# Kernel tuning notes

Hardware: AMD Instinct MI355X
Metric: run time of the kernel (lower is better)

## Reference

```python
import jax, jax.numpy as jnp
import numpy as np

EPS_DIV = 1e-7   # matches .div(sigma + 1e-07) and denominator + 1e-07
EPS_NORM = 1e-12  # torch F.normalize default eps


def setup_inputs() -> dict:
    key = jax.random.key(0)
    k1, k2, k3, k4 = jax.random.split(key, 4)
    B, C, H, W = 4, 128, 64, 64
    K = 32
    stdv = 1.0 / np.sqrt(C)
    return {
        "x": jax.random.normal(k1, (B, C, H, W), dtype=jnp.float32),
        "anchor": jax.random.uniform(k2, (K, C), dtype=jnp.float32),
        "sigma_param": jax.random.uniform(k3, (K, C), dtype=jnp.float32),
        "gcn_weight": jax.random.uniform(k4, (C, C), dtype=jnp.float32,
                                         minval=-stdv, maxval=stdv),
    }


def _l2_normalize(v, axis):
    n = jnp.sqrt(jnp.sum(v * v, axis=axis, keepdims=True))
    return v / jnp.maximum(n, EPS_NORM)


def reference(x, anchor, sigma_param, gcn_weight):
    B, C, H, W = x.shape
    N = H * W
    K = anchor.shape[0]

    # --- GraphNet (NetVLAD-style soft assignment pooling) ---
    sigma = jax.nn.sigmoid(sigma_param)                        # [K, C]
    xf = x.reshape(B, C, N).transpose(0, 2, 1)                 # [B, N, C]
    # residual: [B, K, N, C]
    residual = (xf[:, None, :, :] - anchor[None, :, None, :]) / (
        sigma[None, :, None, :] + EPS_DIV)
    logits = -0.5 * jnp.sum(residual * residual, axis=3)       # [B, K, N]
    soft_assign = jax.nn.softmax(logits, axis=1)               # softmax over nodes K

    numerator = jnp.einsum('bknc,bkn->bkc', residual, soft_assign)  # [B, K, C]
    denominator = jnp.sum(soft_assign, axis=2)[..., None]           # [B, K, 1]
    nodes = numerator / (denominator + EPS_DIV)                     # [B, K, C]

    nodes = _l2_normalize(nodes, axis=2)
    flat = nodes.reshape(B, -1)
    flat = _l2_normalize(flat, axis=1)
    graph = flat.reshape(B, C, K)  # note: pure reshape as in torch .view

    # --- CascadeGCNet, loop = 1 ---
    adj = jnp.einsum('bck,bcl->bkl', graph, graph)             # x_t @ x -> [B, K, K]
    adj = jax.nn.softmax(adj, axis=2)
    support = jnp.einsum('bck,cd->bkd', graph, gcn_weight)     # [B, K, C]
    graph = jnp.einsum('bkl,bld->bkd', adj, support).transpose(0, 2, 1)  # [B, C, K]
    graph = jax.nn.relu(graph)

    # --- project back ---
    out = jnp.einsum('bck,bkn->bcn', graph, soft_assign)       # [B, C, N]
    return out.reshape(B, C, H, W)
```

## Files before the change

kernel.cpp:

```cpp
#include <hip/hip_runtime.h>
#include <math.h>

#define BB 4
#define CC 128
#define KK 32
#define NN 4096
#define NSL 64

__launch_bounds__(1024, 4)
__global__ void k_A(const float* __restrict__ x, const float* __restrict__ anchor,
                    const float* __restrict__ sigp, float* __restrict__ sa,
                    float* __restrict__ pnum, float* __restrict__ pden) {
  const int b  = blockIdx.y, s = blockIdx.x;
  const int n0 = s * 64;
  const int t  = threadIdx.x;
  const int lane = t & 63;
  const int w  = __builtin_amdgcn_readfirstlane(t >> 6);

  __shared__ float  xt[CC][68];
  __shared__ float4 wt4[16][129];
  __shared__ float  plg[4][64][36];
  __shared__ float  stK[KK][68];
  __shared__ float  ckL[KK];
  __shared__ float  pdenP[8][36];

  {
#pragma unroll
    for (int e = 0; e < 2; e++) {
      int i = t + e * 1024;
      int c = i >> 4, pq = i & 15;
      float4 v = *(const float4*)(x + ((size_t)b * CC + c) * NN + n0 + 4 * pq);
      *(float4*)&xt[c][4 * pq] = v;
    }
  }

  {
    const int kp = w;
    const int k0 = kp * 2, k1 = k0 + 1;
    float s0 = 0.f, s1 = 0.f;
#pragma unroll
    for (int e = 0; e < 2; e++) {
      int c = lane * 2 + e;
      float sp0 = sigp[k0 * CC + c], sp1 = sigp[k1 * CC + c];
      float a0  = anchor[k0 * CC + c], a1 = anchor[k1 * CC + c];
      float sg0 = 1.0f / (1.0f + expf(-sp0));
      float sg1 = 1.0f / (1.0f + expf(-sp1));
      float iv0 = 1.0f / (sg0 + 1e-7f), iv1 = 1.0f / (sg1 + 1e-7f);
      float w20 = iv0 * iv0, w21 = iv1 * iv1;
      wt4[kp][c] = make_float4(w20, -2.0f * a0 * w20, w21, -2.0f * a1 * w21);
      s0 = fmaf(a0 * a0, w20, s0);
      s1 = fmaf(a1 * a1, w21, s1);
    }
#pragma unroll
    for (int d = 1; d < 64; d <<= 1) {
      s0 += __shfl_xor(s0, d);
      s1 += __shfl_xor(s1, d);
    }
    if (lane == 0) { ckL[k0] = s0; ckL[k1] = s1; }
  }
  __syncthreads();

  {
    const int px4 = t & 15, kp = (t >> 4) & 15, ch = t >> 8;
    float acc[4][2];
#pragma unroll
    for (int i = 0; i < 4; i++) { acc[i][0] = 0.f; acc[i][1] = 0.f; }
    for (int c0 = 0; c0 < 32; c0++) {
      const int c = ch * 32 + c0;
      float4 xv = *(const float4*)&xt[c][px4 * 4];
      float4 wv = wt4[kp][c];
#pragma unroll
      for (int i = 0; i < 4; i++) {
        float xs = (&xv.x)[i];
        acc[i][0] = fmaf(xs, fmaf(xs, wv.x, wv.y), acc[i][0]);
        acc[i][1] = fmaf(xs, fmaf(xs, wv.z, wv.w), acc[i][1]);
      }
    }
#pragma unroll
    for (int i = 0; i < 4; i++) {
      plg[ch][px4 * 4 + i][kp * 2 + 0] = acc[i][0];
      plg[ch][px4 * 4 + i][kp * 2 + 1] = acc[i][1];
    }
  }
  __syncthreads();

  if (t < 512) {
    const int p  = w * 8 + (lane >> 3);
    const int kq = lane & 7;
    float4 l0  = *(float4*)&plg[0][p][kq * 4];
    float4 l1  = *(float4*)&plg[1][p][kq * 4];
    float4 l2  = *(float4*)&plg[2][p][kq * 4];
    float4 l3  = *(float4*)&plg[3][p][kq * 4];
    float4 ckv = *(float4*)&ckL[kq * 4];
    float4 lv;
    lv.x = -0.5f * (l0.x + l1.x + l2.x + l3.x + ckv.x);
    lv.y = -0.5f * (l0.y + l1.y + l2.y + l3.y + ckv.y);
    lv.z = -0.5f * (l0.z + l1.z + l2.z + l3.z + ckv.z);
    lv.w = -0.5f * (l0.w + l1.w + l2.w + l3.w + ckv.w);
    float m = fmaxf(fmaxf(lv.x, lv.y), fmaxf(lv.z, lv.w));
    m = fmaxf(m, __shfl_xor(m, 1));
    m = fmaxf(m, __shfl_xor(m, 2));
    m = fmaxf(m, __shfl_xor(m, 4));
    float e0 = __expf(lv.x - m), e1 = __expf(lv.y - m);
    float e2 = __expf(lv.z - m), e3 = __expf(lv.w - m);
    float sum = e0 + e1 + e2 + e3;
    sum += __shfl_xor(sum, 1);
    sum += __shfl_xor(sum, 2);
    sum += __shfl_xor(sum, 4);
    float rs = 1.0f / sum;
    e0 *= rs; e1 *= rs; e2 *= rs; e3 *= rs;
    stK[kq * 4 + 0][p] = e0;
    stK[kq * 4 + 1][p] = e1;
    stK[kq * 4 + 2][p] = e2;
    stK[kq * 4 + 3][p] = e3;
    float p0 = e0, p1 = e1, p2 = e2, p3 = e3;
    p0 += __shfl_xor(p0, 8);  p1 += __shfl_xor(p1, 8);
    p2 += __shfl_xor(p2, 8);  p3 += __shfl_xor(p3, 8);
    p0 += __shfl_xor(p0, 16); p1 += __shfl_xor(p1, 16);
    p2 += __shfl_xor(p2, 16); p3 += __shfl_xor(p3, 16);
    p0 += __shfl_xor(p0, 32); p1 += __shfl_xor(p1, 32);
    p2 += __shfl_xor(p2, 32); p3 += __shfl_xor(p3, 32);
    if (lane < 8) {
      pdenP[w][lane * 4 + 0] = p0;
      pdenP[w][lane * 4 + 1] = p1;
      pdenP[w][lane * 4 + 2] = p2;
      pdenP[w][lane * 4 + 3] = p3;
    }
  }
  __syncthreads();

  if (t < KK) {
    float d = 0.f;
#pragma unroll
    for (int ww = 0; ww < 8; ww++) d += pdenP[ww][t];
    pden[((size_t)b * NSL + s) * KK + t] = d;
  }

  if (t < 512) {
    const int k = t >> 4, j4 = t & 15;
    float4 v = *(float4*)&stK[k][4 * j4];
    *(float4*)(sa + ((size_t)b * KK + k) * NN + n0 + 4 * j4) = v;
  }

  {
    const int k = t & 31, cg = t >> 5;
    float acc[4];
#pragma unroll
    for (int i = 0; i < 4; i++) acc[i] = 0.f;
    const float* xb = x + (size_t)(b * CC + cg * 4) * NN + n0;
    for (int j4 = 0; j4 < 16; j4++) {
      float4 sv = *(float4*)&stK[k][4 * j4];
#pragma unroll
      for (int i = 0; i < 4; i++) {
        float4 xr = *(const float4*)(xb + (size_t)i * NN + 4 * j4);
        acc[i] = fmaf(sv.x, xr.x, acc[i]);
        acc[i] = fmaf(sv.y, xr.y, acc[i]);
        acc[i] = fmaf(sv.z, xr.z, acc[i]);
        acc[i] = fmaf(sv.w, xr.w, acc[i]);
      }
    }
    float* pp = pnum + (((size_t)b * NSL + s) * KK + k) * CC + cg * 4;
    *(float4*)pp = make_float4(acc[0], acc[1], acc[2], acc[3]);
  }
}

__launch_bounds__(256)
__global__ void k_red(const float* __restrict__ pnum, const float* __restrict__ pden,
                      const float* __restrict__ sigp, const float* __restrict__ anchor,
                      float* __restrict__ nodes, float* __restrict__ n1sq) {
  const int t = threadIdx.x;
  const int g = blockIdx.x * 256 + t;
  const int c = g & 127, k = (g >> 7) & 31, b = g >> 12;

  float dk = 0.0f;
#pragma unroll 8
  for (int s = 0; s < NSL; s++) dk += pden[((size_t)b * NSL + s) * KK + k];

  float q = 0.0f;
#pragma unroll 8
  for (int s = 0; s < NSL; s++)
    q += pnum[(((size_t)b * NSL + s) * KK + k) * CC + c];

  const int idx = k * CC + c;
  float sg = 1.0f / (1.0f + expf(-sigp[idx]));
  float iv = 1.0f / (sg + 1e-7f);
  float val = iv * (q - anchor[idx] * dk) / (dk + 1e-7f);
  nodes[((size_t)b * KK + k) * CC + c] = val;

  __shared__ float red[256];
  red[t] = val * val;
  __syncthreads();
  for (int sft = 64; sft > 0; sft >>= 1) {
    if ((t & 127) < sft) red[t] += red[t + sft];
    __syncthreads();
  }
  if ((t & 127) == 0) n1sq[b * KK + k] = red[t];
}

__launch_bounds__(1024, 4)
__global__ void k_BC(const float* __restrict__ nodes, const float* __restrict__ n1sq,
                     const float* __restrict__ W, const float* __restrict__ sa,
                     float* __restrict__ out) {
  const int b = blockIdx.y, s = blockIdx.x;
  const int n0 = s * 64;
  const int t = threadIdx.x;
  __shared__ float flat[KK * CC];
  __shared__ float sup[KK][130];
  __shared__ float adjm[KK][33];
  __shared__ float gbL[CC][KK + 1];
  __shared__ float n1v[KK], nsq[KK];
  __shared__ float n2s;

  const int k = t >> 5, cq = t & 31;
  float4 val = ((const float4*)(nodes + (size_t)b * KK * CC))[k * 32 + cq];

  if (t < KK) {
    float s2 = n1sq[b * KK + t];
    float n1 = fmaxf(sqrtf(s2), 1e-12f);
    n1v[t] = n1;
    nsq[t] = s2 / (n1 * n1);
  }
  __syncthreads();
  if (t == 0) {
    float tot = 0.0f;
#pragma unroll
    for (int kk = 0; kk < KK; kk++) tot += nsq[kk];
    n2s = fmaxf(sqrtf(tot), 1e-12f);
  }
  __syncthreads();
  {
    float sc = 1.0f / (n1v[k] * n2s);
    val.x *= sc; val.y *= sc; val.z *= sc; val.w *= sc;
    ((float4*)flat)[k * 32 + cq] = val;
  }
  __syncthreads();

  {
    const int k2 = t >> 5, l = t & 31;
    float a = 0.0f;
#pragma unroll 8
    for (int i = 0; i < CC; i++)
      a = fmaf(flat[i * KK + k2], flat[i * KK + l], a);
    adjm[k2][l] = a;
  }
  __syncthreads();
  if (t < KK) {
    float m = -1e30f;
#pragma unroll
    for (int l = 0; l < KK; l++) m = fmaxf(m, adjm[t][l]);
    float s2 = 0.0f;
#pragma unroll
    for (int l = 0; l < KK; l++) { float e = __expf(adjm[t][l] - m); adjm[t][l] = e; s2 += e; }
    float r = 1.0f / s2;
#pragma unroll
    for (int l = 0; l < KK; l++) adjm[t][l] *= r;
  }
  __syncthreads();

  {
    const int d = t & 127, lg = t >> 7;
    float sacc[4] = {0.0f, 0.0f, 0.0f, 0.0f};
    for (int c = 0; c < CC; c++) {
      float wv = W[c * CC + d];
#pragma unroll
      for (int j = 0; j < 4; j++)
        sacc[j] = fmaf(flat[c * KK + lg + 8 * j], wv, sacc[j]);
    }
#pragma unroll
    for (int j = 0; j < 4; j++) sup[lg + 8 * j][d] = sacc[j];
  }
  __syncthreads();

  {
    const int d = t & 127, lg = t >> 7;
#pragma unroll
    for (int j = 0; j < 4; j++) {
      int kk = lg + 8 * j;
      float g = 0.0f;
#pragma unroll
      for (int l = 0; l < KK; l++) g = fmaf(adjm[kk][l], sup[l][d], g);
      gbL[d][kk] = fmaxf(g, 0.0f);
    }
  }
  __syncthreads();

  {
    const int nl = t & 63, cw = t >> 6;
    const int c0 = cw * 8;
    float sreg[KK];
    const float* spt = sa + (size_t)b * KK * NN + n0 + nl;
#pragma unroll
    for (int kk = 0; kk < KK; kk++) sreg[kk] = spt[(size_t)kk * NN];

    float* op = out + ((size_t)b * CC + c0) * NN + n0 + nl;
#pragma unroll
    for (int ci = 0; ci < 8; ci++) {
      float acc = 0.0f;
#pragma unroll
      for (int kk = 0; kk < KK; kk++)
        acc = fmaf(gbL[c0 + ci][kk], sreg[kk], acc);
      op[(size_t)ci * NN] = acc;
    }
  }
}

extern "C" void kernel_launch(void* const* d_in, const int* in_sizes, int n_in,
                              void* d_out, int out_size, void* d_ws, size_t ws_size,
                              hipStream_t stream) {
  const float* x      = (const float*)d_in[0];
  const float* anchor = (const float*)d_in[1];
  const float* sigp   = (const float*)d_in[2];
  const float* W      = (const float*)d_in[3];
  float* out = (float*)d_out;

  float* ws    = (float*)d_ws;
  float* pden  = ws;
  float* pnum  = ws + 8192;
  float* nodes = ws + 1056768;
  float* n1sq  = ws + 1073152;
  float* sa    = ws + 1073280;

  k_A  <<<dim3(NSL, BB), dim3(1024), 0, stream>>>(x, anchor, sigp, sa, pnum, pden);
  k_red<<<dim3(64),      dim3(256),  0, stream>>>(pnum, pden, sigp, anchor, nodes, n1sq);
  k_BC <<<dim3(NSL, BB), dim3(1024), 0, stream>>>(nodes, n1sq, W, sa, out);
}
```

Measured before the change: 54.29 us.

## Register-tile logits and numerator GEMMs in k_A using transposed LDS copies

The logits stage now uses 256 threads, each computing an 8-pixel by 4-node register tile. The numerator stage reads a transposed x tile and transposed soft-assign from LDS instead of re-reading x from global memory, with 128 threads each computing an 8x8 tile. Partial numerators are now split into two halves per slice, which doubles the pnum workspace and the reduction length in k_red. Most threads sit idle in both compute phases, and the extra LDS buffers, possible bank conflicts on the transposed stores and larger partial-sum traffic may offset the gain from reuse.

Result: slower. 58.11 us (+7.0%).

```diff
diff --git a/kernel.cpp b/kernel.cpp
--- a/kernel.cpp
+++ b/kernel.cpp
@@ -6,6 +6,7 @@
 #define KK 32
 #define NN 4096
 #define NSL 64
+#define NSL2 128
 
 __launch_bounds__(1024, 4)
 __global__ void k_A(const float* __restrict__ x, const float* __restrict__ anchor,
@@ -17,12 +18,14 @@
   const int lane = t & 63;
   const int w  = __builtin_amdgcn_readfirstlane(t >> 6);
 
-  __shared__ float  xt[CC][68];
-  __shared__ float4 wt4[16][129];
-  __shared__ float  plg[4][64][36];
-  __shared__ float  stK[KK][68];
-  __shared__ float  ckL[KK];
-  __shared__ float  pdenP[8][36];
+  __shared__ __align__(16) float  xt[CC][64];
+  __shared__ __align__(16) float  xtT[64][132];
+  __shared__ __align__(16) float4 wt4[16][129];
+  __shared__ __align__(16) float  plg[4][64][36];
+  __shared__ __align__(16) float  stT[64][36];
+  __shared__ __align__(16) float  stK[KK][68];
+  __shared__ __align__(16) float  ckL[KK];
+  __shared__ float pdenP[8][36];
 
   {
 #pragma unroll
@@ -31,6 +34,10 @@
       int c = i >> 4, pq = i & 15;
       float4 v = *(const float4*)(x + ((size_t)b * CC + c) * NN + n0 + 4 * pq);
       *(float4*)&xt[c][4 * pq] = v;
+      xtT[4 * pq + 0][c] = v.x;
+      xtT[4 * pq + 1][c] = v.y;
+      xtT[4 * pq + 2][c] = v.z;
+      xtT[4 * pq + 3][c] = v.w;
     }
   }
 
@@ -60,27 +67,42 @@
   }
   __syncthreads();
 
-  {
-    const int px4 = t & 15, kp = (t >> 4) & 15, ch = t >> 8;
-    float acc[4][2];
-#pragma unroll
-    for (int i = 0; i < 4; i++) { acc[i][0] = 0.f; acc[i][1] = 0.f; }
+  if (t < 256) {
+    const int cs = w;
+    const int pxg = lane & 7, kg = lane >> 3;
+    float acc[8][4];
+#pragma unroll
+    for (int i = 0; i < 8; i++)
+#pragma unroll
+      for (int j = 0; j < 4; j++) acc[i][j] = 0.f;
+
     for (int c0 = 0; c0 < 32; c0++) {
-      const int c = ch * 32 + c0;
-      float4 xv = *(const float4*)&xt[c][px4 * 4];
-      float4 wv = wt4[kp][c];
+      const int c = cs * 32 + c0;
+      float4 xv0 = *(float4*)&xt[c][pxg * 8];
+      float4 xv1 = *(float4*)&xt[c][pxg * 8 + 4];
+      float4 w0  = wt4[kg * 2][c];
+      float4 w1  = wt4[kg * 2 + 1][c];
 #pragma unroll
       for (int i = 0; i < 4; i++) {
-        float xs = (&xv.x)[i];
-        acc[i][0] = fmaf(xs, fmaf(xs, wv.x, wv.y), acc[i][0]);
-        acc[i][1] = fmaf(xs, fmaf(xs, wv.z, wv.w), acc[i][1]);
+        float xs = (&xv0.x)[i];
+        acc[i][0] = fmaf(xs, fmaf(xs, w0.x, w0.y), acc[i][0]);
+        acc[i][1] = fmaf(xs, fmaf(xs, w0.z, w0.w), acc[i][1]);
+        acc[i][2] = fmaf(xs, fmaf(xs, w1.x, w1.y), acc[i][2]);
+        acc[i][3] = fmaf(xs, fmaf(xs, w1.z, w1.w), acc[i][3]);
       }
-    }
-#pragma unroll
-    for (int i = 0; i < 4; i++) {
-      plg[ch][px4 * 4 + i][kp * 2 + 0] = acc[i][0];
-      plg[ch][px4 * 4 + i][kp * 2 + 1] = acc[i][1];
-    }
+#pragma unroll
+      for (int i = 0; i < 4; i++) {
+        float xs = (&xv1.x)[i];
+        acc[4 + i][0] = fmaf(xs, fmaf(xs, w0.x, w0.y), acc[4 + i][0]);
+        acc[4 + i][1] = fmaf(xs, fmaf(xs, w0.z, w0.w), acc[4 + i][1]);
+        acc[4 + i][2] = fmaf(xs, fmaf(xs, w1.x, w1.y), acc[4 + i][2]);
+        acc[4 + i][3] = fmaf(xs, fmaf(xs, w1.z, w1.w), acc[4 + i][3]);
+      }
+    }
+#pragma unroll
+    for (int i = 0; i < 8; i++)
+      *(float4*)&plg[cs][pxg * 8 + i][kg * 4] =
+          make_float4(acc[i][0], acc[i][1], acc[i][2], acc[i][3]);
   }
   __syncthreads();
 
@@ -109,6 +131,7 @@
     sum += __shfl_xor(sum, 4);
     float rs = 1.0f / sum;
     e0 *= rs; e1 *= rs; e2 *= rs; e3 *= rs;
+    *(float4*)&stT[p][kq * 4] = make_float4(e0, e1, e2, e3);
     stK[kq * 4 + 0][p] = e0;
     stK[kq * 4 + 1][p] = e1;
     stK[kq * 4 + 2][p] = e2;
@@ -142,25 +165,37 @@
     *(float4*)(sa + ((size_t)b * KK + k) * NN + n0 + 4 * j4) = v;
   }
 
-  {
-    const int k = t & 31, cg = t >> 5;
-    float acc[4];
-#pragma unroll
-    for (int i = 0; i < 4; i++) acc[i] = 0.f;
-    const float* xb = x + (size_t)(b * CC + cg * 4) * NN + n0;
-    for (int j4 = 0; j4 < 16; j4++) {
-      float4 sv = *(float4*)&stK[k][4 * j4];
-#pragma unroll
-      for (int i = 0; i < 4; i++) {
-        float4 xr = *(const float4*)(xb + (size_t)i * NN + 4 * j4);
-        acc[i] = fmaf(sv.x, xr.x, acc[i]);
-        acc[i] = fmaf(sv.y, xr.y, acc[i]);
-        acc[i] = fmaf(sv.z, xr.z, acc[i]);
-        acc[i] = fmaf(sv.w, xr.w, acc[i]);
-      }
-    }
-    float* pp = pnum + (((size_t)b * NSL + s) * KK + k) * CC + cg * 4;
-    *(float4*)pp = make_float4(acc[0], acc[1], acc[2], acc[3]);
+  if (t >= 512 && t < 640) {
+    const int tt = t - 512;
+    const int kg = tt & 3;
+    const int cg = (tt >> 2) & 15;
+    const int ns = tt >> 6;
+    float acc[8][8];
+#pragma unroll
+    for (int i = 0; i < 8; i++)
+#pragma unroll
+      for (int j = 0; j < 8; j++) acc[i][j] = 0.f;
+
+    for (int p0 = 0; p0 < 32; p0++) {
+      const int px = ns * 32 + p0;
+      float4 s0 = *(float4*)&stT[px][kg * 8];
+      float4 s1 = *(float4*)&stT[px][kg * 8 + 4];
+      float4 x0 = *(float4*)&xtT[px][cg * 8];
+      float4 x1 = *(float4*)&xtT[px][cg * 8 + 4];
+      float sk[8] = {s0.x, s0.y, s0.z, s0.w, s1.x, s1.y, s1.z, s1.w};
+      float xc[8] = {x0.x, x0.y, x0.z, x0.w, x1.x, x1.y, x1.z, x1.w};
+#pragma unroll
+      for (int i = 0; i < 8; i++)
+#pragma unroll
+        for (int j = 0; j < 8; j++)
+          acc[i][j] = fmaf(sk[i], xc[j], acc[i][j]);
+    }
+#pragma unroll
+    for (int i = 0; i < 8; i++) {
+      float* pp = pnum + (((size_t)b * NSL2 + s * 2 + ns) * KK + kg * 8 + i) * CC + cg * 8;
+      *(float4*)pp       = make_float4(acc[i][0], acc[i][1], acc[i][2], acc[i][3]);
+      *(float4*)(pp + 4) = make_float4(acc[i][4], acc[i][5], acc[i][6], acc[i][7]);
+    }
   }
 }
 
@@ -178,8 +213,8 @@
 
   float q = 0.0f;
 #pragma unroll 8
-  for (int s = 0; s < NSL; s++)
-    q += pnum[(((size_t)b * NSL + s) * KK + k) * CC + c];
+  for (int s = 0; s < NSL2; s++)
+    q += pnum[(((size_t)b * NSL2 + s) * KK + k) * CC + c];
 
   const int idx = k * CC + c;
   float sg = 1.0f / (1.0f + expf(-sigp[idx]));
@@ -316,9 +351,9 @@
   float* ws    = (float*)d_ws;
   float* pden  = ws;
   float* pnum  = ws + 8192;
-  float* nodes = ws + 1056768;
-  float* n1sq  = ws + 1073152;
-  float* sa    = ws + 1073280;
+  float* nodes = ws + 2105344;
+  float* n1sq  = ws + 2121728;
+  float* sa    = ws + 2121856;
 
   k_A  <<<dim3(NSL, BB), dim3(1024), 0, stream>>>(x, anchor, sigp, sa, pnum, pden);
   k_red<<<dim3(64),      dim3(256),  0, stream>>>(pnum, pden, sigp, anchor, nodes, n1sq);
```

## Halve k_A pixel slice to 32 with 512-thread blocks, doubling slice count

Applied to the files above, without the earlier changes.

The first kernel now processes 32 pixels per block with 512 threads instead of 64 pixels with 1024, so it launches twice as many blocks (128 slices per batch). The per-node constant reduction changes from wave shuffles to a shared-memory partial sum. The numerator loop now has each thread accumulate 8 channels. The intent is better occupancy and more blocks across CUs. The cost is doubling the partial-sum buffers that k_red must reduce over, while k_BC keeps its own 64-slice grid.

After: 68.42 us. 1.26x slower.

```diff
diff --git a/kernel.cpp b/kernel.cpp
--- a/kernel.cpp
+++ b/kernel.cpp
@@ -5,42 +5,45 @@
 #define CC 128
 #define KK 32
 #define NN 4096
-#define NSL 64
-
-__launch_bounds__(1024, 4)
+#define PX 32
+#define NSL 128
+#define NSLB 64
+
+__launch_bounds__(512, 4)
 __global__ void k_A(const float* __restrict__ x, const float* __restrict__ anchor,
                     const float* __restrict__ sigp, float* __restrict__ sa,
                     float* __restrict__ pnum, float* __restrict__ pden) {
   const int b  = blockIdx.y, s = blockIdx.x;
-  const int n0 = s * 64;
+  const int n0 = s * PX;
   const int t  = threadIdx.x;
   const int lane = t & 63;
   const int w  = __builtin_amdgcn_readfirstlane(t >> 6);
 
-  __shared__ float  xt[CC][68];
-  __shared__ float4 wt4[16][129];
-  __shared__ float  plg[4][64][36];
-  __shared__ float  stK[KK][68];
-  __shared__ float  ckL[KK];
-  __shared__ float  pdenP[8][36];
+  __shared__ __align__(16) float  xt[CC][36];
+  __shared__ __align__(16) float4 wt4[16][128];
+  __shared__ __align__(16) float  plg[4][PX][36];
+  __shared__ __align__(16) float  stK[KK][36];
+  __shared__ __align__(16) float  ckp[KK][33];
+  __shared__ __align__(16) float  ckL[KK];
+  __shared__ float pdenP[4][36];
 
   {
 #pragma unroll
     for (int e = 0; e < 2; e++) {
-      int i = t + e * 1024;
-      int c = i >> 4, pq = i & 15;
+      int i = t + e * 512;
+      int c = i >> 3, pq = i & 7;
       float4 v = *(const float4*)(x + ((size_t)b * CC + c) * NN + n0 + 4 * pq);
       *(float4*)&xt[c][4 * pq] = v;
     }
   }
 
   {
-    const int kp = w;
+    const int kp = t >> 5;
     const int k0 = kp * 2, k1 = k0 + 1;
     float s0 = 0.f, s1 = 0.f;
 #pragma unroll
-    for (int e = 0; e < 2; e++) {
-      int c = lane * 2 + e;
+    for (int e = 0; e < 4; e++) {
+      int c = ((t * 4) + e) & 127;
       float sp0 = sigp[k0 * CC + c], sp1 = sigp[k1 * CC + c];
       float a0  = anchor[k0 * CC + c], a1 = anchor[k1 * CC + c];
       float sg0 = 1.0f / (1.0f + expf(-sp0));
@@ -51,17 +54,20 @@
       s0 = fmaf(a0 * a0, w20, s0);
       s1 = fmaf(a1 * a1, w21, s1);
     }
-#pragma unroll
-    for (int d = 1; d < 64; d <<= 1) {
-      s0 += __shfl_xor(s0, d);
-      s1 += __shfl_xor(s1, d);
-    }
-    if (lane == 0) { ckL[k0] = s0; ckL[k1] = s1; }
-  }
-  __syncthreads();
-
-  {
-    const int px4 = t & 15, kp = (t >> 4) & 15, ch = t >> 8;
+    ckp[k0][t & 31] = s0;
+    ckp[k1][t & 31] = s1;
+  }
+  __syncthreads();
+
+  if (t < KK) {
+    float ssum = 0.f;
+#pragma unroll
+    for (int j = 0; j < 32; j++) ssum += ckp[t][j];
+    ckL[t] = ssum;
+  }
+
+  {
+    const int px4 = t & 7, kp = (t >> 3) & 15, ch = t >> 7;
     float acc[4][2];
 #pragma unroll
     for (int i = 0; i < 4; i++) { acc[i][0] = 0.f; acc[i][1] = 0.f; }
@@ -84,7 +90,7 @@
   }
   __syncthreads();
 
-  if (t < 512) {
+  if (t < 256) {
     const int p  = w * 8 + (lane >> 3);
     const int kq = lane & 7;
     float4 l0  = *(float4*)&plg[0][p][kq * 4];
@@ -132,26 +138,27 @@
   if (t < KK) {
     float d = 0.f;
 #pragma unroll
-    for (int ww = 0; ww < 8; ww++) d += pdenP[ww][t];
+    for (int ww = 0; ww < 4; ww++) d += pdenP[ww][t];
     pden[((size_t)b * NSL + s) * KK + t] = d;
   }
 
-  if (t < 512) {
-    const int k = t >> 4, j4 = t & 15;
+  if (t < 256) {
+    const int k = t >> 3, j4 = t & 7;
     float4 v = *(float4*)&stK[k][4 * j4];
     *(float4*)(sa + ((size_t)b * KK + k) * NN + n0 + 4 * j4) = v;
   }
 
   {
     const int k = t & 31, cg = t >> 5;
-    float acc[4];
-#pragma unroll
-    for (int i = 0; i < 4; i++) acc[i] = 0.f;
-    const float* xb = x + (size_t)(b * CC + cg * 4) * NN + n0;
-    for (int j4 = 0; j4 < 16; j4++) {
+    float acc[8];
+#pragma unroll
+    for (int i = 0; i < 8; i++) acc[i] = 0.f;
+    const float* xb = x + (size_t)(b * CC + cg * 8) * NN + n0;
+#pragma unroll
+    for (int j4 = 0; j4 < 8; j4++) {
       float4 sv = *(float4*)&stK[k][4 * j4];
 #pragma unroll
-      for (int i = 0; i < 4; i++) {
+      for (int i = 0; i < 8; i++) {
         float4 xr = *(const float4*)(xb + (size_t)i * NN + 4 * j4);
         acc[i] = fmaf(sv.x, xr.x, acc[i]);
         acc[i] = fmaf(sv.y, xr.y, acc[i]);
@@ -159,8 +166,9 @@
         acc[i] = fmaf(sv.w, xr.w, acc[i]);
       }
     }
-    float* pp = pnum + (((size_t)b * NSL + s) * KK + k) * CC + cg * 4;
-    *(float4*)pp = make_float4(acc[0], acc[1], acc[2], acc[3]);
+    float* pp = pnum + (((size_t)b * NSL + s) * KK + k) * CC + cg * 8;
+    *(float4*)pp       = make_float4(acc[0], acc[1], acc[2], acc[3]);
+    *(float4*)(pp + 4) = make_float4(acc[4], acc[5], acc[6], acc[7]);
   }
 }
 
@@ -315,12 +323,12 @@
 
   float* ws    = (float*)d_ws;
   float* pden  = ws;
-  float* pnum  = ws + 8192;
-  float* nodes = ws + 1056768;
-  float* n1sq  = ws + 1073152;
-  float* sa    = ws + 1073280;
-
-  k_A  <<<dim3(NSL, BB), dim3(1024), 0, stream>>>(x, anchor, sigp, sa, pnum, pden);
-  k_red<<<dim3(64),      dim3(256),  0, stream>>>(pnum, pden, sigp, anchor, nodes, n1sq);
-  k_BC <<<dim3(NSL, BB), dim3(1024), 0, stream>>>(nodes, n1sq, W, sa, out);
+  float* pnum  = ws + 16384;
+  float* nodes = ws + 2113536;
+  float* n1sq  = ws + 2129920;
+  float* sa    = ws + 2130048;
+
+  k_A  <<<dim3(NSL, BB),  dim3(512),  0, stream>>>(x, anchor, sigp, sa, pnum, pden);
+  k_red<<<dim3(64),       dim3(256),  0, stream>>>(pnum, pden, sigp, anchor, nodes, n1sq);
+  k_BC <<<dim3(NSLB, BB), dim3(1024), 0, stream>>>(nodes, n1sq, W, sa, out);
 }
```

## Fuse partial-sum reduction into the graph kernel, dropping the separate reduction launch

Applied to the files above, without the earlier changes.

Removes the standalone reduction kernel. Each block of the graph/projection kernel now reduces the per-slice numerator and denominator partials itself, computes the nodes, and forms their L2 norms in shared memory. This saves one kernel launch and the nodes/norm round trip through global memory. In exchange, every block redundantly re-reads all partial numerators for its batch, which multiplies cache traffic many times over.

New measurement: 58.94 us. 1.09x slower.

```diff
diff --git a/kernel.cpp b/kernel.cpp
--- a/kernel.cpp
+++ b/kernel.cpp
@@ -164,43 +164,11 @@
   }
 }
 
-__launch_bounds__(256)
-__global__ void k_red(const float* __restrict__ pnum, const float* __restrict__ pden,
+__launch_bounds__(1024, 4)
+__global__ void k_BCR(const float* __restrict__ pnum, const float* __restrict__ pden,
                       const float* __restrict__ sigp, const float* __restrict__ anchor,
-                      float* __restrict__ nodes, float* __restrict__ n1sq) {
-  const int t = threadIdx.x;
-  const int g = blockIdx.x * 256 + t;
-  const int c = g & 127, k = (g >> 7) & 31, b = g >> 12;
-
-  float dk = 0.0f;
-#pragma unroll 8
-  for (int s = 0; s < NSL; s++) dk += pden[((size_t)b * NSL + s) * KK + k];
-
-  float q = 0.0f;
-#pragma unroll 8
-  for (int s = 0; s < NSL; s++)
-    q += pnum[(((size_t)b * NSL + s) * KK + k) * CC + c];
-
-  const int idx = k * CC + c;
-  float sg = 1.0f / (1.0f + expf(-sigp[idx]));
-  float iv = 1.0f / (sg + 1e-7f);
-  float val = iv * (q - anchor[idx] * dk) / (dk + 1e-7f);
-  nodes[((size_t)b * KK + k) * CC + c] = val;
-
-  __shared__ float red[256];
-  red[t] = val * val;
-  __syncthreads();
-  for (int sft = 64; sft > 0; sft >>= 1) {
-    if ((t & 127) < sft) red[t] += red[t + sft];
-    __syncthreads();
-  }
-  if ((t & 127) == 0) n1sq[b * KK + k] = red[t];
-}
-
-__launch_bounds__(1024, 4)
-__global__ void k_BC(const float* __restrict__ nodes, const float* __restrict__ n1sq,
-                     const float* __restrict__ W, const float* __restrict__ sa,
-                     float* __restrict__ out) {
+                      const float* __restrict__ W, const float* __restrict__ sa,
+                      float* __restrict__ out) {
   const int b = blockIdx.y, s = blockIdx.x;
   const int n0 = s * 64;
   const int t = threadIdx.x;
@@ -208,21 +176,66 @@
   __shared__ float sup[KK][130];
   __shared__ float adjm[KK][33];
   __shared__ float gbL[CC][KK + 1];
-  __shared__ float n1v[KK], nsq[KK];
+  __shared__ float redp[32][33];
+  __shared__ float denl[KK], n1v[KK], nsq[KK];
   __shared__ float n2s;
 
   const int k = t >> 5, cq = t & 31;
-  float4 val = ((const float4*)(nodes + (size_t)b * KK * CC))[k * 32 + cq];
-
+
+  {
+    const int sg = t >> 5, kk = t & 31;
+    redp[sg][kk] = pden[((size_t)b * NSL + sg) * KK + kk]
+                 + pden[((size_t)b * NSL + 32 + sg) * KK + kk];
+  }
+
+  float4 q = make_float4(0.f, 0.f, 0.f, 0.f);
+  {
+    const float4* p4 = (const float4*)pnum + (size_t)b * NSL * (KK * CC / 4)
+                     + k * 32 + cq;
+#pragma unroll 8
+    for (int ss = 0; ss < NSL; ss++) {
+      float4 v = p4[(size_t)ss * (KK * CC / 4)];
+      q.x += v.x; q.y += v.y; q.z += v.z; q.w += v.w;
+    }
+  }
+  __syncthreads();
   if (t < KK) {
-    float s2 = n1sq[b * KK + t];
+    float d = 0.f;
+#pragma unroll
+    for (int sg = 0; sg < 32; sg++) d += redp[sg][t];
+    denl[t] = d;
+  }
+  __syncthreads();
+
+  float4 val;
+  {
+    const float dk = denl[k];
+    const float rden = 1.0f / (dk + 1e-7f);
+    const int idx4 = k * 32 + cq;
+    float4 sp = ((const float4*)sigp)[idx4];
+    float4 av = ((const float4*)anchor)[idx4];
+    float iv0 = 1.0f / (1.0f / (1.0f + expf(-sp.x)) + 1e-7f);
+    float iv1 = 1.0f / (1.0f / (1.0f + expf(-sp.y)) + 1e-7f);
+    float iv2 = 1.0f / (1.0f / (1.0f + expf(-sp.z)) + 1e-7f);
+    float iv3 = 1.0f / (1.0f / (1.0f + expf(-sp.w)) + 1e-7f);
+    val.x = iv0 * (q.x - av.x * dk) * rden;
+    val.y = iv1 * (q.y - av.y * dk) * rden;
+    val.z = iv2 * (q.z - av.z * dk) * rden;
+    val.w = iv3 * (q.w - av.w * dk) * rden;
+    redp[cq][k] = val.x * val.x + val.y * val.y + val.z * val.z + val.w * val.w;
+  }
+  __syncthreads();
+  if (t < KK) {
+    float s2 = 0.f;
+#pragma unroll
+    for (int j = 0; j < 32; j++) s2 += redp[j][t];
     float n1 = fmaxf(sqrtf(s2), 1e-12f);
     n1v[t] = n1;
     nsq[t] = s2 / (n1 * n1);
   }
   __syncthreads();
   if (t == 0) {
-    float tot = 0.0f;
+    float tot = 0.f;
 #pragma unroll
     for (int kk = 0; kk < KK; kk++) tot += nsq[kk];
     n2s = fmaxf(sqrtf(tot), 1e-12f);
@@ -313,14 +326,11 @@
   const float* W      = (const float*)d_in[3];
   float* out = (float*)d_out;
 
-  float* ws    = (float*)d_ws;
-  float* pden  = ws;
-  float* pnum  = ws + 8192;
-  float* nodes = ws + 1056768;
-  float* n1sq  = ws + 1073152;
-  float* sa    = ws + 1073280;
+  float* ws   = (float*)d_ws;
+  float* pden = ws;
+  float* pnum = ws + 8192;
+  float* sa   = ws + 1056768;
 
   k_A  <<<dim3(NSL, BB), dim3(1024), 0, stream>>>(x, anchor, sigp, sa, pnum, pden);
-  k_red<<<dim3(64),      dim3(256),  0, stream>>>(pnum, pden, sigp, anchor, nodes, n1sq);
-  k_BC <<<dim3(NSL, BB), dim3(1024), 0, stream>>>(nodes, n1sq, W, sa, out);
+  k_BCR<<<dim3(NSL, BB), dim3(1024), 0, stream>>>(pnum, pden, sigp, anchor, W, sa, out);
 }
```
